# Kernel optimization log

Hardware: AMD Instinct MI355X
Metric: run time of the kernel (lower is better)

## Reference

```python
import jax, jax.numpy as jnp
import numpy as np

B, S, V, E, H, O = 256, 128, 50000, 256, 512, 32


def _cell(x, h, c, Wih, Whh, bih, bhh):
    # PyTorch LSTM gate order: i, f, g, o
    g = x @ Wih.T + h @ Whh.T + bih + bhh
    i, f, gg, o = jnp.split(g, 4, axis=-1)
    c = jax.nn.sigmoid(f) * c + jax.nn.sigmoid(i) * jnp.tanh(gg)
    h = jax.nn.sigmoid(o) * jnp.tanh(c)
    return h, c


def setup_inputs() -> dict:
    key = jax.random.key(0)
    ks = iter(jax.random.split(key, 32))
    n = lambda shape: jax.random.normal(next(ks), shape, dtype=jnp.float32) * 0.05
    return {
        'x': jax.random.randint(next(ks), (B, S), 0, V),
        'emb': n((V, E)),
        'enc_Wih0': n((4 * H, E)), 'enc_Whh0': n((4 * H, H)),
        'enc_bih0': n((4 * H,)), 'enc_bhh0': n((4 * H,)),
        'enc_Wih1': n((4 * H, H)), 'enc_Whh1': n((4 * H, H)),
        'enc_bih1': n((4 * H,)), 'enc_bhh1': n((4 * H,)),
        'dec_Wih0': n((4 * H, O)), 'dec_Whh0': n((4 * H, H)),
        'dec_bih0': n((4 * H,)), 'dec_bhh0': n((4 * H,)),
        'dec_Wih1': n((4 * H, H)), 'dec_Whh1': n((4 * H, H)),
        'dec_bih1': n((4 * H,)), 'dec_bhh1': n((4 * H,)),
        'fc_w': n((S, O, H)), 'fc_b': n((S, O)),
    }


def reference(x, emb, enc_Wih0, enc_Whh0, enc_bih0, enc_bhh0,
              enc_Wih1, enc_Whh1, enc_bih1, enc_bhh1,
              dec_Wih0, dec_Whh0, dec_bih0, dec_bhh0,
              dec_Wih1, dec_Whh1, dec_bih1, dec_bhh1,
              fc_w, fc_b):
    b = x.shape[0]
    xe = jnp.swapaxes(emb[x], 0, 1)  # [S, B, E]
    z = jnp.zeros((b, H), jnp.float32)

    # 2-layer LSTM encoder (eval mode: no dropout)
    def enc0(carry, xi):
        h, c = _cell(xi, carry[0], carry[1], enc_Wih0, enc_Whh0, enc_bih0, enc_bhh0)
        return (h, c), h
    (h0, c0), y0 = jax.lax.scan(enc0, (z, z), xe)

    def enc1(carry, xi):
        h, c = _cell(xi, carry[0], carry[1], enc_Wih1, enc_Whh1, enc_bih1, enc_bhh1)
        return (h, c), h
    (h1, c1), _ = jax.lax.scan(enc1, (z, z), y0)

    # greedy decoder: one-hot of previous argmax fed back each step
    in0 = jnp.zeros((b, O), jnp.float32).at[:, 0].set(1.0)

    def dec(carry, wb):
        h0, c0, h1, c1, xin = carry
        w, bb = wb  # per-step Linear: w [O, H], bb [O]
        h0, c0 = _cell(xin, h0, c0, dec_Wih0, dec_Whh0, dec_bih0, dec_bhh0)
        h1, c1 = _cell(h0, h1, c1, dec_Wih1, dec_Whh1, dec_bih1, dec_bhh1)
        probs = jax.nn.softmax(h1 @ w.T + bb, axis=-1)  # [B, O]
        nxt = jax.nn.one_hot(jnp.argmax(probs, axis=-1), O, dtype=probs.dtype)
        return (h0, c0, h1, c1, nxt), probs

    _, out = jax.lax.scan(dec, (h0, c0, h1, c1, in0), (fc_w, fc_b))
    return jnp.swapaxes(out, 0, 1)  # [B, S, O]
```

## Files before the change

### kernel.cpp

```cpp
#include <hip/hip_runtime.h>


#define BN 256
#define SN 128
#define EN 256
#define HN 512
#define ON 32
#define RG 32
#define NCG 32
#define NTHREADS 256
#define XSTR 264
#define HSTR 520
#define FSTR 520
#define GSTR 68
#define POLL_GUARD (1 << 20)

typedef _Float16 f16;
typedef _Float16 f16x8 __attribute__((ext_vector_type(8)));
typedef _Float16 f16x2 __attribute__((ext_vector_type(2)));
typedef float f32x4 __attribute__((ext_vector_type(4)));
typedef unsigned u32x4 __attribute__((ext_vector_type(4)));

__device__ __forceinline__ f32x4 MFMA16(f16x8 a, f16x8 b, f32x4 c) {
  return __builtin_amdgcn_mfma_f32_16x16x32_f16(a, b, c, 0, 0, 0);
}

__device__ __forceinline__ float sigf(float x) { return 1.0f / (1.0f + __expf(-x)); }

template<int NKT>
__device__ __forceinline__ void loadW(const float* __restrict__ Wb, int K, int col, int quad,
                                      f16x8* dst) {
  #pragma unroll
  for (int kt = 0; kt < NKT; ++kt) {
    const float* p = Wb + (size_t)col * K + kt * 32 + quad * 8;
    f32x4 a = *(const f32x4*)p;
    f32x4 b = *(const f32x4*)(p + 4);
    f16x8 h;
    h[0] = (f16)a[0]; h[1] = (f16)a[1]; h[2] = (f16)a[2]; h[3] = (f16)a[3];
    h[4] = (f16)b[0]; h[5] = (f16)b[1]; h[6] = (f16)b[2]; h[7] = (f16)b[3];
    dst[kt] = h;
  }
}

__device__ __forceinline__ void issue8(u32x4* v, const char* __restrict__ src, int tid) {
  const char* base = src + tid * 16;
  #pragma unroll
  for (int j = 0; j < 8; ++j)
    asm volatile("global_load_dwordx4 %0, %1, off sc1" : "=v"(v[j]) : "v"(base + j * 4096));
}
__device__ __forceinline__ void write8(f16* dst, const u32x4* v, int tid) {
  #pragma unroll
  for (int j = 0; j < 8; ++j) {
    int u = j * 256 + tid, rr = u >> 6, cc = u & 63;
    *(u32x4*)&dst[rr * HSTR + cc * 8] = v[j];
  }
}

template<int NKT>
__device__ __forceinline__ void matmulAcc(f32x4* acc, const f16* stage, int stride,
                                          const f16x8* Wr, int l16, int quad) {
  #pragma unroll
  for (int mt = 0; mt < 2; ++mt) {
    #pragma unroll
    for (int kt = 0; kt < NKT; ++kt) {
      f16x8 a = *(const f16x8*)&stage[(mt * 16 + l16) * stride + kt * 32 + quad * 8];
      acc[mt] = MFMA16(a, Wr[kt], acc[mt]);
    }
  }
}

__device__ __forceinline__ void arrive_ctr(int* slots, int g, int tid) {
  __syncthreads();
  if (tid == 0) {
    asm volatile("s_waitcnt vmcnt(0)" ::: "memory");
    int one = 1;
    int* p = &slots[g * 64 + 40];
    asm volatile("global_atomic_add %0, %1, off" :: "v"(p), "v"(one) : "memory");
  }
}

__device__ __forceinline__ void wait_ctr(int* slots, int g, int target, int* esc) {
  if (!*esc) {
    const int* p = &slots[g * 64 + 40];
    int gd = 0;
    for (;;) {
      int v = __hip_atomic_load(p, __ATOMIC_RELAXED, __HIP_MEMORY_SCOPE_AGENT);
      if (v >= target) break;
      if (++gd > POLL_GUARD) { *esc = 1; break; }
      __builtin_amdgcn_s_sleep(1);
    }
  }
  asm volatile("" ::: "memory");
}

__device__ __forceinline__ void gatherXE(f16* xes, const int* __restrict__ xTok,
                                         const float* __restrict__ emb, int g, int k, int tid) {
  int r = tid >> 3, sub = tid & 7;
  int tok = xTok[(g * RG + r) * SN + k];
  const float* er = emb + (size_t)tok * EN + sub * 32;
  f16* dst = &xes[r * XSTR + sub * 32];
  #pragma unroll
  for (int jj = 0; jj < 32; jj += 8) {
    f32x4 a = *(const f32x4*)(er + jj);
    f32x4 b = *(const f32x4*)(er + jj + 4);
    f16x8 hv;
    hv[0] = (f16)a[0]; hv[1] = (f16)a[1]; hv[2] = (f16)a[2]; hv[3] = (f16)a[3];
    hv[4] = (f16)b[0]; hv[5] = (f16)b[1]; hv[6] = (f16)b[2]; hv[7] = (f16)b[3];
    *(f16x8*)(dst + jj) = hv;
  }
}

__device__ __forceinline__ void stageFCW(f16* fcwb, const float* __restrict__ fcw,
                                         int st, int tid) {
  int col = tid >> 3, k0 = (tid & 7) * 64;
  const float* src = fcw + ((size_t)st * ON + col) * HN + k0;
  f16* dstp = &fcwb[col * FSTR + k0];
  #pragma unroll
  for (int jj = 0; jj < 64; jj += 8) {
    f32x4 a = *(const f32x4*)(src + jj);
    f32x4 b = *(const f32x4*)(src + jj + 4);
    f16x8 hv;
    hv[0] = (f16)a[0]; hv[1] = (f16)a[1]; hv[2] = (f16)a[2]; hv[3] = (f16)a[3];
    hv[4] = (f16)b[0]; hv[5] = (f16)b[1]; hv[6] = (f16)b[2]; hv[7] = (f16)b[3];
    *(f16x8*)(dstp + jj) = hv;
  }
}

__device__ __forceinline__ void pointwise_store(const float* gb, int row, int d0, float* cv,
                                                unsigned* __restrict__ hout, int g, int cg,
                                                int sub) {
  const float* gr = gb + row * GSTR + d0;
  union { unsigned u; f16x2 h; } hv;
  #pragma unroll
  for (int j = 0; j < 2; ++j) {
    float vi = gr[j], vf = gr[16 + j], vg = gr[32 + j], vo = gr[48 + j];
    cv[j] = sigf(vf) * cv[j] + sigf(vi) * tanhf(vg);
    hv.h[j] = (f16)(sigf(vo) * tanhf(cv[j]));
  }
  __hip_atomic_store(&hout[(g * RG + row) * 256 + cg * 8 + sub], hv.u,
                     __ATOMIC_RELAXED, __HIP_MEMORY_SCOPE_AGENT);
}

__launch_bounds__(NTHREADS, 1)
__global__ void lstm_all(const int* __restrict__ xTok, const float* __restrict__ emb,
    const float* __restrict__ eWih0, const float* __restrict__ eWhh0,
    const float* __restrict__ ebih0, const float* __restrict__ ebhh0,
    const float* __restrict__ eWih1, const float* __restrict__ eWhh1,
    const float* __restrict__ ebih1, const float* __restrict__ ebhh1,
    const float* __restrict__ dWih0, const float* __restrict__ dWhh0,
    const float* __restrict__ dbih0, const float* __restrict__ dbhh0,
    const float* __restrict__ dWih1, const float* __restrict__ dWhh1,
    const float* __restrict__ dbih1, const float* __restrict__ dbhh1,
    const float* __restrict__ fcw, const float* __restrict__ fcb,
    float* __restrict__ dout, char* __restrict__ h0buf, char* __restrict__ h1buf,
    int* __restrict__ slots)
{
  __shared__ __align__(16) char upool[RG * XSTR * 2];
  __shared__ __align__(16) f16 h0s[RG * HSTR];
  __shared__ __align__(16) f16 h1s[RG * HSTR];
  __shared__ __align__(16) f16 fcwb[ON * FSTR];
  __shared__ float gbuf0[RG * GSTR];
  __shared__ float gbuf1[RG * GSTR];
  __shared__ int amaxlds[RG];
  __shared__ int esc;

  f16*   xes  = (f16*)upool;
  float* lbuf = (float*)upool;
  float* w0d  = (float*)(upool + 4352);

  const int tid  = threadIdx.x;
  const int g    = blockIdx.x & 7;
  const int cg   = blockIdx.x >> 3;
  const int w    = tid >> 6;
  const int lane = tid & 63;
  const int quad = lane >> 4;
  const int l16  = lane & 15;
  const int colg = w * HN + cg * 16 + l16;
  const int urow = tid >> 3;
  const int ud0  = (tid & 7) * 2;
  int ctarget = 0;
  if (tid == 0) esc = 0;

  f16x8 Wi0r[8], Wh0r[16], Wi1r[16], Wh1r[16];
  loadW<8>(eWih0, EN, colg, quad, Wi0r);
  loadW<16>(eWhh0, HN, colg, quad, Wh0r);
  loadW<16>(eWih1, HN, colg, quad, Wi1r);
  loadW<16>(eWhh1, HN, colg, quad, Wh1r);
  float bias0 = ebih0[colg] + ebhh0[colg];
  float bias1 = ebih1[colg] + ebhh1[colg];

  gatherXE(xes, xTok, emb, g, 0, tid);
  float c0[2] = {0.f, 0.f}, c1[2] = {0.f, 0.f};
  {
    unsigned idx = (unsigned)(BN * 256 + (g * RG + urow) * 256 + cg * 8 + (tid & 7));
    __hip_atomic_store((unsigned*)h0buf + idx, 0u, __ATOMIC_RELAXED, __HIP_MEMORY_SCOPE_AGENT);
    __hip_atomic_store((unsigned*)h1buf + idx, 0u, __ATOMIC_RELAXED, __HIP_MEMORY_SCOPE_AGENT);
  }
  __syncthreads();
  if (tid == 0) {
    __hip_atomic_store(&slots[g * 64 + 40], 0, __ATOMIC_RELAXED, __HIP_MEMORY_SCOPE_AGENT);
    asm volatile("s_waitcnt vmcnt(0)" ::: "memory");
    __hip_atomic_store(&slots[g * 64 + cg], 1, __ATOMIC_RELAXED, __HIP_MEMORY_SCOPE_AGENT);
  }
  if (!esc) {
    int idx = tid & 31;
    int gd = 0;
    for (;;) {
      int v = __hip_atomic_load(&slots[g * 64 + idx], __ATOMIC_RELAXED, __HIP_MEMORY_SCOPE_AGENT);
      if (__all(v >= 1)) break;
      if (++gd > POLL_GUARD) { esc = 1; break; }
      __builtin_amdgcn_s_sleep(1);
    }
  }
  __syncthreads();

  for (int k = 0; k <= SN; ++k) {
    u32x4 v0[8], v1[8];
    issue8(v0, h0buf + (size_t)((k - 1) & 1) * BN * HN * 2 + (size_t)(g * RG) * HN * 2, tid);
    if (k >= 1)
      issue8(v1, h1buf + (size_t)(k & 1) * BN * HN * 2 + (size_t)(g * RG) * HN * 2, tid);

    f32x4 acc0[2], acc1[2];
    if (k < SN) {
      f32x4 b0; b0[0] = bias0; b0[1] = bias0; b0[2] = bias0; b0[3] = bias0;
      acc0[0] = b0; acc0[1] = b0;
      matmulAcc<8>(acc0, xes, XSTR, Wi0r, l16, quad);
    }
    if (k >= 1) asm volatile("s_waitcnt vmcnt(8)" ::: "memory");
    else        asm volatile("s_waitcnt vmcnt(0)" ::: "memory");
    write8(h0s, v0, tid);
    __syncthreads();
    if (k < SN) matmulAcc<16>(acc0, h0s, HSTR, Wh0r, l16, quad);
    if (k >= 1) {
      f32x4 b1; b1[0] = bias1; b1[1] = bias1; b1[2] = bias1; b1[3] = bias1;
      acc1[0] = b1; acc1[1] = b1;
      matmulAcc<16>(acc1, h0s, HSTR, Wi1r, l16, quad);
      asm volatile("s_waitcnt vmcnt(0)" ::: "memory");
      write8(h1s, v1, tid);
      __syncthreads();
      matmulAcc<16>(acc1, h1s, HSTR, Wh1r, l16, quad);
    }

    #pragma unroll
    for (int mt = 0; mt < 2; ++mt) {
      #pragma unroll
      for (int i = 0; i < 4; ++i) {
        int rr = (mt * 16 + quad * 4 + i) * GSTR + w * 16 + l16;
        if (k < SN) gbuf0[rr] = acc0[mt][i];
        if (k >= 1) gbuf1[rr] = acc1[mt][i];
      }
    }
    __syncthreads();
    if (k < SN)
      pointwise_store(gbuf0, urow, ud0, c0,
                      (unsigned*)(h0buf + (size_t)(k & 1) * BN * HN * 2), g, cg, tid & 7);
    if (k >= 1)
      pointwise_store(gbuf1, urow, ud0, c1,
                      (unsigned*)(h1buf + (size_t)((k - 1) & 1) * BN * HN * 2), g, cg, tid & 7);

    arrive_ctr(slots, g, tid);
    if (k < SN - 1) gatherXE(xes, xTok, emb, g, k + 1, tid);
    __syncthreads();
    ctarget += NCG;
    wait_ctr(slots, g, ctarget, &esc);
  }

  loadW<16>(dWhh0, HN, colg, quad, Wh0r);
  loadW<16>(dWih1, HN, colg, quad, Wi1r);
  loadW<16>(dWhh1, HN, colg, quad, Wh1r);
  bias0 = dbih0[colg] + dbhh0[colg];
  bias1 = dbih1[colg] + dbhh1[colg];
  {
    int cl = tid >> 2, i0 = (tid & 3) * 8;
    int gcol = (cl >> 4) * HN + cg * 16 + (cl & 15);
    const float* p = dWih0 + (size_t)gcol * ON + i0;
    #pragma unroll
    for (int j = 0; j < 8; ++j) w0d[cl * 32 + i0 + j] = p[j];
  }
  if (tid < RG) amaxlds[tid] = 0;

  for (int t = 0; t <= SN; ++t) {
    u32x4 v0[8];
    issue8(v0, h1buf + (size_t)((t - 1) & 1) * BN * HN * 2 + (size_t)(g * RG) * HN * 2, tid);
    float fb = 0.f;
    if (t >= 1) fb = fcb[(t - 1) * ON + ((w >> 1) * 16 + l16)];

    f32x4 acc0[2];
    if (t < SN) {
      acc0[0] = f32x4{0.f, 0.f, 0.f, 0.f}; acc0[1] = acc0[0];
      matmulAcc<16>(acc0, h0s, HSTR, Wh0r, l16, quad);
    }
    asm volatile("s_waitcnt vmcnt(0)" ::: "memory");
    write8(h1s, v0, tid);
    __syncthreads();

    if (t >= 1) {
      int fmt = w & 1, fnt = w >> 1;
      int colo = fnt * 16 + l16;
      f32x4 afc = {0.f, 0.f, 0.f, 0.f};
      #pragma unroll
      for (int kt = 0; kt < 16; ++kt) {
        f16x8 bf = *(const f16x8*)&fcwb[colo * FSTR + kt * 32 + quad * 8];
        f16x8 av = *(const f16x8*)&h1s[(fmt * 16 + l16) * HSTR + kt * 32 + quad * 8];
        afc = MFMA16(av, bf, afc);
      }
      #pragma unroll
      for (int i = 0; i < 4; ++i)
        lbuf[(fmt * 16 + quad * 4 + i) * 33 + colo] = afc[i] + fb;
      __syncthreads();
      {
        int st = t - 1;
        int row = tid >> 3, s = tid & 7, cbase = s * 4;
        float vv[4];
        #pragma unroll
        for (int j = 0; j < 4; ++j) vv[j] = lbuf[row * 33 + cbase + j];
        float mx = vv[0]; int bi = cbase;
        #pragma unroll
        for (int j = 1; j < 4; ++j)
          if (vv[j] > mx) { mx = vv[j]; bi = cbase + j; }
        #pragma unroll
        for (int m = 1; m < 8; m <<= 1) {
          float om = __shfl_xor(mx, m);
          int   ob = __shfl_xor(bi, m);
          if (om > mx || (om == mx && ob < bi)) { mx = om; bi = ob; }
        }
        float e[4], ss = 0.f;
        #pragma unroll
        for (int j = 0; j < 4; ++j) { e[j] = __expf(vv[j] - mx); ss += e[j]; }
        #pragma unroll
        for (int m = 1; m < 8; m <<= 1) ss += __shfl_xor(ss, m);
        if (s == 0) amaxlds[row] = bi;
        if (cg == 0) {
          float inv = 1.0f / ss;
          float* op = dout + ((size_t)(g * RG + row) * SN + st) * ON + cbase;
          #pragma unroll
          for (int j = 0; j < 4; ++j) op[j] = e[j] * inv;
        }
      }
      __syncthreads();
    }

    if (t < SN) {
      #pragma unroll
      for (int mt = 0; mt < 2; ++mt) {
        #pragma unroll
        for (int i = 0; i < 4; ++i) {
          int row = mt * 16 + quad * 4 + i;
          acc0[mt][i] += bias0 + w0d[(w * 16 + l16) * 32 + amaxlds[row]];
        }
      }
      #pragma unroll
      for (int mt = 0; mt < 2; ++mt) {
        #pragma unroll
        for (int i = 0; i < 4; ++i)
          gbuf0[(mt * 16 + quad * 4 + i) * GSTR + w * 16 + l16] = acc0[mt][i];
      }
      __syncthreads();
      pointwise_store(gbuf0, urow, ud0, c0,
                      (unsigned*)(h0buf + (size_t)(t & 1) * BN * HN * 2), g, cg, tid & 7);
    }
    arrive_ctr(slots, g, tid);
    ctarget += NCG;
    wait_ctr(slots, g, ctarget, &esc);

    if (t < SN) {
      u32x4 v2[8];
      issue8(v2, h0buf + (size_t)(t & 1) * BN * HN * 2 + (size_t)(g * RG) * HN * 2, tid);
      f32x4 acc1[2];
      f32x4 b1; b1[0] = bias1; b1[1] = bias1; b1[2] = bias1; b1[3] = bias1;
      acc1[0] = b1; acc1[1] = b1;
      matmulAcc<16>(acc1, h1s, HSTR, Wh1r, l16, quad);
      asm volatile("s_waitcnt vmcnt(0)" ::: "memory");
      write8(h0s, v2, tid);
      __syncthreads();
      matmulAcc<16>(acc1, h0s, HSTR, Wi1r, l16, quad);
      #pragma unroll
      for (int mt = 0; mt < 2; ++mt) {
        #pragma unroll
        for (int i = 0; i < 4; ++i)
          gbuf0[(mt * 16 + quad * 4 + i) * GSTR + w * 16 + l16] = acc1[mt][i];
      }
      __syncthreads();
      pointwise_store(gbuf0, urow, ud0, c1,
                      (unsigned*)(h1buf + (size_t)(t & 1) * BN * HN * 2), g, cg, tid & 7);
      arrive_ctr(slots, g, tid);
      stageFCW(fcwb, fcw, t, tid);
      __syncthreads();
      ctarget += NCG;
      wait_ctr(slots, g, ctarget, &esc);
    }
  }
}

extern "C" void kernel_launch(void* const* d_in, const int* in_sizes, int n_in,
                              void* d_out, int out_size, void* d_ws, size_t ws_size,
                              hipStream_t stream) {
  (void)in_sizes; (void)n_in; (void)out_size; (void)ws_size;
  const int*   xTok  = (const int*)d_in[0];
  const float* emb   = (const float*)d_in[1];
  const float* eWih0 = (const float*)d_in[2];
  const float* eWhh0 = (const float*)d_in[3];
  const float* ebih0 = (const float*)d_in[4];
  const float* ebhh0 = (const float*)d_in[5];
  const float* eWih1 = (const float*)d_in[6];
  const float* eWhh1 = (const float*)d_in[7];
  const float* ebih1 = (const float*)d_in[8];
  const float* ebhh1 = (const float*)d_in[9];
  const float* dWih0 = (const float*)d_in[10];
  const float* dWhh0 = (const float*)d_in[11];
  const float* dbih0 = (const float*)d_in[12];
  const float* dbhh0 = (const float*)d_in[13];
  const float* dWih1 = (const float*)d_in[14];
  const float* dWhh1 = (const float*)d_in[15];
  const float* dbih1 = (const float*)d_in[16];
  const float* dbhh1 = (const float*)d_in[17];
  const float* fcw   = (const float*)d_in[18];
  const float* fcb   = (const float*)d_in[19];

  char* h0buf = (char*)d_ws;
  char* h1buf = (char*)d_ws + (size_t)2 * BN * HN * 2;
  int*  slots = (int*)((char*)d_ws + (size_t)4 * BN * HN * 2);

  hipLaunchKernelGGL(lstm_all, dim3(256), dim3(NTHREADS), 0, stream,
                     xTok, emb, eWih0, eWhh0, ebih0, ebhh0, eWih1, eWhh1, ebih1, ebhh1,
                     dWih0, dWhh0, dbih0, dbhh0, dWih1, dWhh1, dbih1, dbhh1,
                     fcw, fcb, (float*)d_out, h0buf, h1buf, slots);
}
```

Baseline: 2.409 ms.

## Replace atomic-add group barrier with per-block round flags and coalesce staging loads

Swaps the shared atomic counter barrier among the 32 blocks of a group for per-block flag slots written with a round number. Each waiter polls all 32 flags in one wavefront vote, and the slots alternate between two banks by round parity. The goal is to remove contention from serialized atomic adds on one address and to have every thread drain its outstanding stores before the barrier. The embedding gather and the fc_w staging loops are also re-indexed for more coalesced global reads, at the cost of wider polling traffic.

```diff
diff --git a/kernel.cpp b/kernel.cpp
--- a/kernel.cpp
+++ b/kernel.cpp
@@ -14,9 +14,11 @@
 #define FSTR 520
 #define GSTR 68
 #define POLL_GUARD (1 << 20)
+#define SLB 128
 
 typedef _Float16 f16;
 typedef _Float16 f16x8 __attribute__((ext_vector_type(8)));
+typedef _Float16 f16x4 __attribute__((ext_vector_type(4)));
 typedef _Float16 f16x2 __attribute__((ext_vector_type(2)));
 typedef float f32x4 __attribute__((ext_vector_type(4)));
 typedef unsigned u32x4 __attribute__((ext_vector_type(4)));
@@ -69,23 +71,21 @@
   }
 }
 
-__device__ __forceinline__ void arrive_ctr(int* slots, int g, int tid) {
+__device__ __forceinline__ void arrive_flag(int* slots, int g, int cg, int tid, int rnd) {
+  asm volatile("s_waitcnt vmcnt(0)" ::: "memory");
   __syncthreads();
-  if (tid == 0) {
-    asm volatile("s_waitcnt vmcnt(0)" ::: "memory");
-    int one = 1;
-    int* p = &slots[g * 64 + 40];
-    asm volatile("global_atomic_add %0, %1, off" :: "v"(p), "v"(one) : "memory");
-  }
-}
-
-__device__ __forceinline__ void wait_ctr(int* slots, int g, int target, int* esc) {
+  if (tid == 0)
+    __hip_atomic_store(&slots[g * SLB + ((rnd & 1) ? 64 : 96) + cg], rnd,
+                       __ATOMIC_RELAXED, __HIP_MEMORY_SCOPE_AGENT);
+}
+
+__device__ __forceinline__ void wait_flag(int* slots, int g, int tid, int rnd, int* esc) {
   if (!*esc) {
-    const int* p = &slots[g * 64 + 40];
+    const int* p = &slots[g * SLB + ((rnd & 1) ? 64 : 96) + (tid & 31)];
     int gd = 0;
     for (;;) {
       int v = __hip_atomic_load(p, __ATOMIC_RELAXED, __HIP_MEMORY_SCOPE_AGENT);
-      if (v >= target) break;
+      if (__all(v == rnd)) break;
       if (++gd > POLL_GUARD) { *esc = 1; break; }
       __builtin_amdgcn_s_sleep(1);
     }
@@ -95,7 +95,7 @@
 
 __device__ __forceinline__ void gatherXE(f16* xes, const int* __restrict__ xTok,
                                          const float* __restrict__ emb, int g, int k, int tid) {
-  int r = tid >> 3, sub = tid & 7;
+  int r = tid & 31, sub = tid >> 5;
   int tok = xTok[(g * RG + r) * SN + k];
   const float* er = emb + (size_t)tok * EN + sub * 32;
   f16* dst = &xes[r * XSTR + sub * 32];
@@ -112,17 +112,15 @@
 
 __device__ __forceinline__ void stageFCW(f16* fcwb, const float* __restrict__ fcw,
                                          int st, int tid) {
-  int col = tid >> 3, k0 = (tid & 7) * 64;
-  const float* src = fcw + ((size_t)st * ON + col) * HN + k0;
-  f16* dstp = &fcwb[col * FSTR + k0];
-  #pragma unroll
-  for (int jj = 0; jj < 64; jj += 8) {
-    f32x4 a = *(const f32x4*)(src + jj);
-    f32x4 b = *(const f32x4*)(src + jj + 4);
-    f16x8 hv;
+  const float* base = fcw + (size_t)st * ON * HN;
+  #pragma unroll
+  for (int j = 0; j < 16; ++j) {
+    int fo = (tid + j * 256) * 4;
+    int col = fo >> 9, k = fo & 511;
+    f32x4 a = *(const f32x4*)(base + fo);
+    f16x4 hv;
     hv[0] = (f16)a[0]; hv[1] = (f16)a[1]; hv[2] = (f16)a[2]; hv[3] = (f16)a[3];
-    hv[4] = (f16)b[0]; hv[5] = (f16)b[1]; hv[6] = (f16)b[2]; hv[7] = (f16)b[3];
-    *(f16x8*)(dstp + jj) = hv;
+    *(f16x4*)&fcwb[col * FSTR + k] = hv;
   }
 }
 
@@ -178,7 +176,7 @@
   const int colg = w * HN + cg * 16 + l16;
   const int urow = tid >> 3;
   const int ud0  = (tid & 7) * 2;
-  int ctarget = 0;
+  int rnd = 0;
   if (tid == 0) esc = 0;
 
   f16x8 Wi0r[8], Wh0r[16], Wi1r[16], Wh1r[16];
@@ -196,17 +194,20 @@
     __hip_atomic_store((unsigned*)h0buf + idx, 0u, __ATOMIC_RELAXED, __HIP_MEMORY_SCOPE_AGENT);
     __hip_atomic_store((unsigned*)h1buf + idx, 0u, __ATOMIC_RELAXED, __HIP_MEMORY_SCOPE_AGENT);
   }
+  asm volatile("s_waitcnt vmcnt(0)" ::: "memory");
   __syncthreads();
   if (tid == 0) {
-    __hip_atomic_store(&slots[g * 64 + 40], 0, __ATOMIC_RELAXED, __HIP_MEMORY_SCOPE_AGENT);
+    __hip_atomic_store(&slots[g * SLB + 64 + cg], 0, __ATOMIC_RELAXED, __HIP_MEMORY_SCOPE_AGENT);
+    __hip_atomic_store(&slots[g * SLB + 96 + cg], 0, __ATOMIC_RELAXED, __HIP_MEMORY_SCOPE_AGENT);
     asm volatile("s_waitcnt vmcnt(0)" ::: "memory");
-    __hip_atomic_store(&slots[g * 64 + cg], 1, __ATOMIC_RELAXED, __HIP_MEMORY_SCOPE_AGENT);
+    __hip_atomic_store(&slots[g * SLB + cg], 1, __ATOMIC_RELAXED, __HIP_MEMORY_SCOPE_AGENT);
   }
   if (!esc) {
     int idx = tid & 31;
     int gd = 0;
     for (;;) {
-      int v = __hip_atomic_load(&slots[g * 64 + idx], __ATOMIC_RELAXED, __HIP_MEMORY_SCOPE_AGENT);
+      int v = __hip_atomic_load(&slots[g * SLB + idx], __ATOMIC_RELAXED,
+                                __HIP_MEMORY_SCOPE_AGENT);
       if (__all(v >= 1)) break;
       if (++gd > POLL_GUARD) { esc = 1; break; }
       __builtin_amdgcn_s_sleep(1);
@@ -258,11 +259,11 @@
       pointwise_store(gbuf1, urow, ud0, c1,
                       (unsigned*)(h1buf + (size_t)((k - 1) & 1) * BN * HN * 2), g, cg, tid & 7);
 
-    arrive_ctr(slots, g, tid);
+    ++rnd;
+    arrive_flag(slots, g, cg, tid, rnd);
     if (k < SN - 1) gatherXE(xes, xTok, emb, g, k + 1, tid);
     __syncthreads();
-    ctarget += NCG;
-    wait_ctr(slots, g, ctarget, &esc);
+    wait_flag(slots, g, tid, rnd, &esc);
   }
 
   loadW<16>(dWhh0, HN, colg, quad, Wh0r);
@@ -359,9 +360,9 @@
       pointwise_store(gbuf0, urow, ud0, c0,
                       (unsigned*)(h0buf + (size_t)(t & 1) * BN * HN * 2), g, cg, tid & 7);
     }
-    arrive_ctr(slots, g, tid);
-    ctarget += NCG;
-    wait_ctr(slots, g, ctarget, &esc);
+    ++rnd;
+    arrive_flag(slots, g, cg, tid, rnd);
+    wait_flag(slots, g, tid, rnd, &esc);
 
     if (t < SN) {
       u32x4 v2[8];
@@ -383,11 +384,11 @@
       __syncthreads();
       pointwise_store(gbuf0, urow, ud0, c1,
                       (unsigned*)(h1buf + (size_t)(t & 1) * BN * HN * 2), g, cg, tid & 7);
-      arrive_ctr(slots, g, tid);
+      ++rnd;
+      arrive_flag(slots, g, cg, tid, rnd);
       stageFCW(fcwb, fcw, t, tid);
       __syncthreads();
-      ctarget += NCG;
-      wait_ctr(slots, g, ctarget, &esc);
+      wait_flag(slots, g, tid, rnd, &esc);
     }
   }
 }
```

Result: slower. 2.922 ms (+21.3%).
